# Kernel optimization log

Hardware: AMD Instinct MI355X
Metric: run time of the kernel (lower is better)

## Reference

```python
import jax, jax.numpy as jnp
import numpy as np

TOP_K = 2
NUM_EXPERTS = 8
D_MODEL = 1024
G, S = 8, 2048


def setup_inputs() -> dict:
    key = jax.random.key(0)
    k1, k2 = jax.random.split(key)
    x = jax.random.normal(k1, (G, S, D_MODEL), dtype=jnp.float32)
    # orthogonal init approximated by scaled normal (same distributional scale);
    gate_weight = jax.random.normal(k2, (D_MODEL, NUM_EXPERTS), dtype=jnp.float32) * (1.0 / np.sqrt(D_MODEL))
    gate_bias = jnp.zeros((1, 1, NUM_EXPERTS), dtype=jnp.float32)
    return {"x": x, "gate_weight": gate_weight, "gate_bias": gate_bias, "expert_capacity": 256}


def reference(x, gate_weight, gate_bias, expert_capacity):
    # gating: (g,s,d) @ (d,e) -> (g,s,e)
    gating_logits = jnp.einsum('gsd,de->gse', x, gate_weight) + gate_bias
    gating_probs = jax.nn.softmax(gating_logits, axis=-1)
    # eval path: exact top-k over experts
    expert_gate, expert_index = jax.lax.top_k(gating_probs, TOP_K)  # (g,s,t)
    expert_mask = jax.nn.one_hot(expert_index, NUM_EXPERTS, dtype=gating_probs.dtype)  # (g,s,t,e)
    # running position of each token within each expert's buffer (1-indexed where assigned)
    position_in_expert = jnp.cumsum(expert_mask, axis=1) * expert_mask  # (g,s,t,e)
    valid_assignment = (position_in_expert < expert_capacity).astype(expert_gate.dtype)
    expert_gate_valid = expert_gate[..., None] * valid_assignment  # (g,s,t,e)
    # one-hot over capacity slots: (g,s,t,e,c)
    slot_one_hot = jax.nn.one_hot(position_in_expert, expert_capacity, dtype=gating_probs.dtype)
    combine_per_assignment = expert_gate_valid[..., None] * slot_one_hot
    combine_tensor = jnp.sum(combine_per_assignment, axis=2)  # contract over t: (g,s,e,c)
    combine_tensor = combine_tensor[..., 1:]  # drop slot 0 (= unassigned)
    dispatch_mask = combine_tensor.astype(bool)
    return (combine_tensor, dispatch_mask)
```

## Files before the change

### kernel.cpp

```cpp
#include <hip/hip_runtime.h>

#define G 8
#define S 2048
#define DMODEL 1024
#define NE 8
#define TOKENS (G * S)

__global__ __launch_bounds__(64) void gate_topk_kernel(
    const float* __restrict__ x, const float* __restrict__ W,
    const float* __restrict__ bias,
    int* __restrict__ idx01, float* __restrict__ g0out,
    float* __restrict__ g1out) {
  const int lane = threadIdx.x;
  const int tok0 = blockIdx.x * 8;

  const float4* W4 = (const float4*)W;
  float4 wa[4][4], wb[4][4];
#pragma unroll
  for (int c = 0; c < 4; ++c) {
#pragma unroll
    for (int j = 0; j < 4; ++j) {
      int d = 4 * (lane + (c << 6)) + j;
      wa[c][j] = W4[d * 2];
      wb[c][j] = W4[d * 2 + 1];
    }
  }
  float b[8];
#pragma unroll
  for (int e = 0; e < 8; ++e) b[e] = bias[e];

  for (int t = 0; t < 8; ++t) {
    const int tok = tok0 + t;
    const float4* xp = (const float4*)(x + (size_t)tok * DMODEL);
    float acc[8] = {0.f, 0.f, 0.f, 0.f, 0.f, 0.f, 0.f, 0.f};
#pragma unroll
    for (int c = 0; c < 4; ++c) {
      float4 xv = xp[lane + (c << 6)];
      const float xs[4] = {xv.x, xv.y, xv.z, xv.w};
#pragma unroll
      for (int j = 0; j < 4; ++j) {
        float s = xs[j];
        acc[0] = fmaf(s, wa[c][j].x, acc[0]);
        acc[1] = fmaf(s, wa[c][j].y, acc[1]);
        acc[2] = fmaf(s, wa[c][j].z, acc[2]);
        acc[3] = fmaf(s, wa[c][j].w, acc[3]);
        acc[4] = fmaf(s, wb[c][j].x, acc[4]);
        acc[5] = fmaf(s, wb[c][j].y, acc[5]);
        acc[6] = fmaf(s, wb[c][j].z, acc[6]);
        acc[7] = fmaf(s, wb[c][j].w, acc[7]);
      }
    }
#pragma unroll
    for (int e = 0; e < 8; ++e) {
      float v = acc[e];
#pragma unroll
      for (int off = 1; off < 64; off <<= 1) v += __shfl_xor(v, off);
      acc[e] = v + b[e];
    }
    if (lane == 0) {
      float m = acc[0];
#pragma unroll
      for (int e = 1; e < 8; ++e) m = fmaxf(m, acc[e]);
      float p[8], sum = 0.f;
#pragma unroll
      for (int e = 0; e < 8; ++e) {
        p[e] = __expf(acc[e] - m);
        sum += p[e];
      }
      int i0 = 0;
      float best = acc[0];
#pragma unroll
      for (int e = 1; e < 8; ++e)
        if (acc[e] > best) { best = acc[e]; i0 = e; }
      int i1 = -1;
      float b1 = 0.f;
#pragma unroll
      for (int e = 0; e < 8; ++e) {
        if (e == i0) continue;
        if (i1 < 0 || acc[e] > b1) { b1 = acc[e]; i1 = e; }
      }
      float inv = 1.0f / sum;
      idx01[tok] = i0 | (i1 << 8);
      g0out[tok] = p[i0] * inv;
      g1out[tok] = p[i1] * inv;
    }
  }
}

__global__ __launch_bounds__(256) void scan_meta_kernel(
    const int* __restrict__ idx01, const float* __restrict__ g0,
    const float* __restrict__ g1, int2* __restrict__ meta, int slots) {
  const int g = blockIdx.x;
  const int t = threadIdx.x;
  const int lane = t & 63;
  const int wave = t >> 6;
  const int base = g * S + t * 8;

  int loc[8];
  unsigned long long a0 = 0ULL, a1 = 0ULL, b0 = 0ULL, b1 = 0ULL;
#pragma unroll
  for (int i = 0; i < 8; ++i) {
    int v = idx01[base + i];
    loc[i] = v;
    int i0 = v & 0xFF, i1 = (v >> 8) & 0xFF;
    if (i0 < 4) a0 += 1ULL << (16 * i0); else a1 += 1ULL << (16 * (i0 & 3));
    if (i1 < 4) b0 += 1ULL << (16 * i1); else b1 += 1ULL << (16 * (i1 & 3));
  }
  const unsigned long long la0 = a0, la1 = a1, lb0 = b0, lb1 = b1;

#pragma unroll
  for (int off = 1; off < 64; off <<= 1) {
    unsigned long long u0 = __shfl_up(a0, (unsigned)off);
    unsigned long long u1 = __shfl_up(a1, (unsigned)off);
    unsigned long long u2 = __shfl_up(b0, (unsigned)off);
    unsigned long long u3 = __shfl_up(b1, (unsigned)off);
    if (lane >= off) { a0 += u0; a1 += u1; b0 += u2; b1 += u3; }
  }

  __shared__ unsigned long long wt[4][4];
  if (lane == 63) {
    wt[wave][0] = a0; wt[wave][1] = a1; wt[wave][2] = b0; wt[wave][3] = b1;
  }
  __syncthreads();
  for (int w = 0; w < wave; ++w) {
    a0 += wt[w][0]; a1 += wt[w][1]; b0 += wt[w][2]; b1 += wt[w][3];
  }

  a0 -= la0; a1 -= la1; b0 -= lb0; b1 -= lb1;

#pragma unroll
  for (int i = 0; i < 8; ++i) {
    const int tok = base + i;
    int v = loc[i];
    int i0 = v & 0xFF, i1 = (v >> 8) & 0xFF;
    int p0, p1;
    {
      int sh = 16 * (i0 & 3);
      if (i0 < 4) { p0 = (int)((a0 >> sh) & 0xFFFF) + 1; a0 += 1ULL << sh; }
      else        { p0 = (int)((a1 >> sh) & 0xFFFF) + 1; a1 += 1ULL << sh; }
    }
    {
      int sh = 16 * (i1 & 3);
      if (i1 < 4) { p1 = (int)((b0 >> sh) & 0xFFFF) + 1; b0 += 1ULL << sh; }
      else        { p1 = (int)((b1 >> sh) & 0xFFFF) + 1; b1 += 1ULL << sh; }
    }
    const float G0 = g0[tok], G1 = g1[tok];
    int2* mrow = meta + (size_t)tok * NE;
#pragma unroll
    for (int e = 0; e < 8; ++e) {
      int tgt = -1;
      float gv = 0.f;
      if (e == i0) {
        if (p0 <= slots) { tgt = p0 - 1; gv = G0; }
      } else if (e == i1) {
        if (p1 <= slots) { tgt = p1 - 1; gv = G1; }
      }
      mrow[e] = make_int2(tgt, __float_as_int(gv));
    }
  }
}

__global__ __launch_bounds__(256) void fill_kernel(
    const int2* __restrict__ meta, float* __restrict__ combine,
    float* __restrict__ dispatch, int nchunks, int total_rows, int slots) {
  const int stride = gridDim.x * 256;
  for (int idx = blockIdx.x * 256 + threadIdx.x; idx < nchunks; idx += stride) {
    const unsigned f = (unsigned)idx * 4u;
    const unsigned row = __umulhi(f, 0x80808081u) >> 7;
    const int sb = (int)(f - row * 255u);
    const int2 mA = meta[row];
    unsigned rB = row + 1u;
    if ((int)rB >= total_rows) rB = row;
    const int2 mB = meta[rB];
    const int ta = mA.x, tb = mB.x;
    const float ga = __int_as_float(mA.y), gb = __int_as_float(mB.y);

    float4 cv;
    {
      int s0 = sb + 0;
      cv.x = (s0 < 255) ? ((s0 == ta) ? ga : 0.f) : ((s0 - 255 == tb) ? gb : 0.f);
      int s1 = sb + 1;
      cv.y = (s1 < 255) ? ((s1 == ta) ? ga : 0.f) : ((s1 - 255 == tb) ? gb : 0.f);
      int s2 = sb + 2;
      cv.z = (s2 < 255) ? ((s2 == ta) ? ga : 0.f) : ((s2 - 255 == tb) ? gb : 0.f);
      int s3 = sb + 3;
      cv.w = (s3 < 255) ? ((s3 == ta) ? ga : 0.f) : ((s3 - 255 == tb) ? gb : 0.f);
    }
    ((float4*)combine)[idx] = cv;
    float4 dv;
    dv.x = (cv.x != 0.f) ? 1.f : 0.f;
    dv.y = (cv.y != 0.f) ? 1.f : 0.f;
    dv.z = (cv.z != 0.f) ? 1.f : 0.f;
    dv.w = (cv.w != 0.f) ? 1.f : 0.f;
    ((float4*)dispatch)[idx] = dv;
  }
}

extern "C" void kernel_launch(void* const* d_in, const int* in_sizes, int n_in,
                              void* d_out, int out_size, void* d_ws,
                              size_t ws_size, hipStream_t stream) {
  const float* x = (const float*)d_in[0];
  const float* W = (const float*)d_in[1];
  const float* bias = (const float*)d_in[2];

  float* out = (float*)d_out;
  const int rows = TOKENS * NE;
  const int slots = out_size / (2 * rows);
  float* combine = out;
  float* dispatch = out + (size_t)(out_size / 2);

  char* ws = (char*)d_ws;
  int* idx01 = (int*)(ws + 0);
  float* g0 = (float*)(ws + TOKENS * 4);
  float* g1 = (float*)(ws + TOKENS * 8);
  int2* meta = (int2*)(ws + TOKENS * 12);

  const int ndwords = rows * slots;
  const int nchunks = ndwords >> 2;

  gate_topk_kernel<<<TOKENS / 8, 64, 0, stream>>>(x, W, bias, idx01, g0, g1);
  scan_meta_kernel<<<G, 256, 0, stream>>>(idx01, g0, g1, meta, slots);
  fill_kernel<<<2048, 256, 0, stream>>>(meta, combine, dispatch, nchunks, rows,
                                        slots);
}
```

Baseline: 335.0 us.

## Zero-fill outputs alongside gating, then scatter nonzero combine/dispatch entries

Replaces the meta-table plus dense fill pass with two steps. The output is zero-filled by extra blocks that run in the same launch as the gating GEMV, and the scan kernel then writes only the assigned slots directly. This removes the meta buffer round-trip and the per-element select logic in the fill, and lets the memory-bound zero fill overlap with gate compute. The gating kernel also moves from one wave per block to four waves per block. The risk is that the scatter writes now depend on the zero fill finishing first, which relies on stream ordering between the two launches.

```diff
diff --git a/kernel.cpp b/kernel.cpp
--- a/kernel.cpp
+++ b/kernel.cpp
@@ -5,14 +5,26 @@
 #define DMODEL 1024
 #define NE 8
 #define TOKENS (G * S)
+#define GATE_BLOCKS 512
+#define FILL_BLOCKS 8192
 
-__global__ __launch_bounds__(64) void gate_topk_kernel(
+__global__ __launch_bounds__(256) void gate_zerofill_kernel(
     const float* __restrict__ x, const float* __restrict__ W,
-    const float* __restrict__ bias,
-    int* __restrict__ idx01, float* __restrict__ g0out,
-    float* __restrict__ g1out) {
-  const int lane = threadIdx.x;
-  const int tok0 = blockIdx.x * 8;
+    const float* __restrict__ bias, int* __restrict__ idx01,
+    float* __restrict__ g0out, float* __restrict__ g1out,
+    float4* __restrict__ out4, int nchunks_total) {
+  if (blockIdx.x >= GATE_BLOCKS) {
+    const int fidx = blockIdx.x - GATE_BLOCKS;
+    const float4 z = make_float4(0.f, 0.f, 0.f, 0.f);
+    const int stride = FILL_BLOCKS * 256;
+    for (int i = fidx * 256 + threadIdx.x; i < nchunks_total; i += stride)
+      out4[i] = z;
+    return;
+  }
+
+  const int lane = threadIdx.x & 63;
+  const int wave = threadIdx.x >> 6;
+  const int tok0 = blockIdx.x * 32 + wave * 8;
 
   const float4* W4 = (const float4*)W;
   float4 wa[4][4], wb[4][4];
@@ -87,9 +99,10 @@
   }
 }
 
-__global__ __launch_bounds__(256) void scan_meta_kernel(
+__global__ __launch_bounds__(256) void scan_scatter_kernel(
     const int* __restrict__ idx01, const float* __restrict__ g0,
-    const float* __restrict__ g1, int2* __restrict__ meta, int slots) {
+    const float* __restrict__ g1, float* __restrict__ combine,
+    float* __restrict__ dispatch, int slots) {
   const int g = blockIdx.x;
   const int t = threadIdx.x;
   const int lane = t & 63;
@@ -144,55 +157,16 @@
       if (i1 < 4) { p1 = (int)((b0 >> sh) & 0xFFFF) + 1; b0 += 1ULL << sh; }
       else        { p1 = (int)((b1 >> sh) & 0xFFFF) + 1; b1 += 1ULL << sh; }
     }
-    const float G0 = g0[tok], G1 = g1[tok];
-    int2* mrow = meta + (size_t)tok * NE;
-#pragma unroll
-    for (int e = 0; e < 8; ++e) {
-      int tgt = -1;
-      float gv = 0.f;
-      if (e == i0) {
-        if (p0 <= slots) { tgt = p0 - 1; gv = G0; }
-      } else if (e == i1) {
-        if (p1 <= slots) { tgt = p1 - 1; gv = G1; }
-      }
-      mrow[e] = make_int2(tgt, __float_as_int(gv));
+    if (p0 <= slots) {
+      size_t off0 = (size_t)(tok * NE + i0) * (size_t)slots + (size_t)(p0 - 1);
+      combine[off0] = g0[tok];
+      dispatch[off0] = 1.f;
     }
-  }
-}
-
-__global__ __launch_bounds__(256) void fill_kernel(
-    const int2* __restrict__ meta, float* __restrict__ combine,
-    float* __restrict__ dispatch, int nchunks, int total_rows, int slots) {
-  const int stride = gridDim.x * 256;
-  for (int idx = blockIdx.x * 256 + threadIdx.x; idx < nchunks; idx += stride) {
-    const unsigned f = (unsigned)idx * 4u;
-    const unsigned row = __umulhi(f, 0x80808081u) >> 7;
-    const int sb = (int)(f - row * 255u);
-    const int2 mA = meta[row];
-    unsigned rB = row + 1u;
-    if ((int)rB >= total_rows) rB = row;
-    const int2 mB = meta[rB];
-    const int ta = mA.x, tb = mB.x;
-    const float ga = __int_as_float(mA.y), gb = __int_as_float(mB.y);
-
-    float4 cv;
-    {
-      int s0 = sb + 0;
-      cv.x = (s0 < 255) ? ((s0 == ta) ? ga : 0.f) : ((s0 - 255 == tb) ? gb : 0.f);
-      int s1 = sb + 1;
-      cv.y = (s1 < 255) ? ((s1 == ta) ? ga : 0.f) : ((s1 - 255 == tb) ? gb : 0.f);
-      int s2 = sb + 2;
-      cv.z = (s2 < 255) ? ((s2 == ta) ? ga : 0.f) : ((s2 - 255 == tb) ? gb : 0.f);
-      int s3 = sb + 3;
-      cv.w = (s3 < 255) ? ((s3 == ta) ? ga : 0.f) : ((s3 - 255 == tb) ? gb : 0.f);
+    if (p1 <= slots) {
+      size_t off1 = (size_t)(tok * NE + i1) * (size_t)slots + (size_t)(p1 - 1);
+      combine[off1] = g1[tok];
+      dispatch[off1] = 1.f;
     }
-    ((float4*)combine)[idx] = cv;
-    float4 dv;
-    dv.x = (cv.x != 0.f) ? 1.f : 0.f;
-    dv.y = (cv.y != 0.f) ? 1.f : 0.f;
-    dv.z = (cv.z != 0.f) ? 1.f : 0.f;
-    dv.w = (cv.w != 0.f) ? 1.f : 0.f;
-    ((float4*)dispatch)[idx] = dv;
   }
 }
 
@@ -213,13 +187,11 @@
   int* idx01 = (int*)(ws + 0);
   float* g0 = (float*)(ws + TOKENS * 4);
   float* g1 = (float*)(ws + TOKENS * 8);
-  int2* meta = (int2*)(ws + TOKENS * 12);
 
-  const int ndwords = rows * slots;
-  const int nchunks = ndwords >> 2;
+  const int nchunks_total = out_size >> 2;
 
-  gate_topk_kernel<<<TOKENS / 8, 64, 0, stream>>>(x, W, bias, idx01, g0, g1);
-  scan_meta_kernel<<<G, 256, 0, stream>>>(idx01, g0, g1, meta, slots);
-  fill_kernel<<<2048, 256, 0, stream>>>(meta, combine, dispatch, nchunks, rows,
-                                        slots);
+  gate_zerofill_kernel<<<GATE_BLOCKS + FILL_BLOCKS, 256, 0, stream>>>(
+      x, W, bias, idx01, g0, g1, (float4*)out, nchunks_total);
+  scan_scatter_kernel<<<G, 256, 0, stream>>>(idx01, g0, g1, combine, dispatch,
+                                             slots);
 }
```

Measured after the change: 338.1 us. Within noise of the previous version (+0.9%).
